# Performance work log

Hardware: AMD Instinct MI355X
Metric: run time of the kernel (lower is better)

## Reference

```python
import jax, jax.numpy as jnp
import numpy as np

B, Z, A = 1024, 512, 8          # batch_size, z_dim, action_dim
AH, ZH = 64, 512                # action_hidden_dim, z_hidden_dim
N_NEG = 100                     # n_neg_actions
TEMP = 0.1                      # temperature
TOP_K = (1, 3, 10)


def forward_model(z, a, Wa, ba, W1, b1, W2, b2):
    # MLP forward model with skip connection (z_delta=True):
    # embed action, concat with z, 2-layer MLP predicting a delta.
    h_a = jax.nn.relu(a @ Wa + ba)                                   # [..., AH]
    h = jax.nn.relu(jnp.concatenate([jnp.broadcast_to(z, a.shape[:-1] + (Z,)), h_a], axis=-1) @ W1 + b1)  # [..., ZH]
    delta = h @ W2 + b2                                              # [..., Z]
    return z + delta


def setup_inputs() -> dict:
    key = jax.random.key(0)
    ks = jax.random.split(key, 8)
    def w(k, shape, fan_in):
        return jax.random.normal(k, shape, jnp.float32) / np.float32(np.sqrt(fan_in))
    z = jax.random.normal(ks[0], (B, Z), jnp.float32)
    z_next = jax.random.normal(ks[1], (B, Z), jnp.float32)
    z_next_hat = jax.random.normal(ks[2], (B, Z), jnp.float32)
    actions = jax.random.normal(ks[3], (B, A), jnp.float32)
    Wa = w(ks[4], (A, AH), A)
    ba = jnp.zeros((AH,), jnp.float32)
    W1 = w(ks[5], (Z + AH, ZH), Z + AH)
    b1 = jnp.zeros((ZH,), jnp.float32)
    W2 = w(ks[6], (ZH, Z), ZH)
    b2 = jnp.zeros((Z,), jnp.float32)
    return {"z": z, "z_next": z_next, "z_next_hat": z_next_hat, "actions": actions,
            "Wa": Wa, "ba": ba, "W1": W1, "b1": b1, "W2": W2, "b2": b2}


def reference(z, z_next, z_next_hat, actions, Wa, ba, W1, b1, W2, b2):
    # ControlCPC.compute_loss with dot_product_similarity, vectorized:
    # the Python loop over n_neg_actions rolled-action forward-model calls
    # becomes one batched [n-1, B, ...] forward-model evaluation.
    batch = z.shape[0]
    n = min(N_NEG, batch)
    sim = z_next @ z_next_hat.T                                      # [B, B] positives on diagonal
    shifts = jnp.arange(1, n)
    neg_actions = jax.vmap(lambda i: jnp.roll(actions, -i, axis=0))(shifts)  # [n-1, B, A]
    z_hat_neg = forward_model(z[None], neg_actions, Wa, ba, W1, b1, W2, b2)  # [n-1, B, Z]
    neg_sim = jnp.einsum('nbz,bz->bn', z_hat_neg, z_next)            # diag of similarity per shift
    sim_mat = jnp.concatenate([sim, neg_sim], axis=1)                # [B, B+n-1]
    # INCE loss, positives on diagonal
    logp = jax.nn.log_softmax(sim_mat / jnp.float32(TEMP), axis=1)
    loss = -jnp.mean(jnp.diagonal(logp))                             # diagonal takes first B entries
    labels = jnp.arange(batch)[:, None]
    accs = []
    for k in TOP_K:
        _, preds = jax.lax.top_k(sim_mat, k)                         # [B, k]
        accs.append(jnp.mean((preds == labels).astype(jnp.float32)) * k)
    return (loss, accs[0], accs[1], accs[2])
```

## Files before the change

kernel.cpp:

```cpp
#include <hip/hip_runtime.h>
#include <math.h>

#define B_SZ 1024
#define Z_DIM 512
#define A_DIM 8
#define AH 64
#define ZH 512
#define NNEG 99
#define INV_T 10.0f

typedef __attribute__((ext_vector_type(8))) short short8;
typedef __attribute__((ext_vector_type(4))) float f32x4;

__device__ __forceinline__ void cvt8(float4 x0, float4 x1, short8& hi, short8& lo) {
    float xs[8] = {x0.x, x0.y, x0.z, x0.w, x1.x, x1.y, x1.z, x1.w};
#pragma unroll
    for (int i = 0; i < 8; ++i) {
        unsigned uu = __float_as_uint(xs[i]);
        hi[i] = (short)(uu >> 16);
        float hf = __uint_as_float(uu & 0xffff0000u);
        lo[i] = (short)(__float_as_uint(xs[i] - hf) >> 16);
    }
}

__device__ __forceinline__ int sw(int m, int kb) { return m * 8 + (kb ^ (m & 7)); }

__global__ __launch_bounds__(256) void prep_kernel(
    const float* __restrict__ W1, const float* __restrict__ actions,
    const float* __restrict__ Wa, const float* __restrict__ ba,
    float* __restrict__ W1T, float* __restrict__ ha, unsigned* __restrict__ cnt)
{
    const int id = blockIdx.x, tid = threadIdx.x;
    if (id == 0 && tid == 0) atomicExch(cnt, 0u);
    if (id < 72) {
        __shared__ float L[64][68];
        int kt = id >> 3, nt = id & 7;
#pragma unroll
        for (int i = 0; i < 4; ++i) {
            int f = tid + i * 256;
            int r = f >> 4, c4 = (f & 15) << 2;
            *(float4*)&L[r][c4] = *(const float4*)&W1[(kt * 64 + r) * 512 + nt * 64 + c4];
        }
        __syncthreads();
#pragma unroll
        for (int i = 0; i < 4; ++i) {
            int f = tid + i * 256;
            int r = f >> 4, c4 = (f & 15) << 2;
            float4 o = {L[c4][r], L[c4 + 1][r], L[c4 + 2][r], L[c4 + 3][r]};
            *(float4*)&W1T[(nt * 64 + r) * 576 + kt * 64 + c4] = o;
        }
    } else if (id < 88) {
        __shared__ float sWa[A_DIM * 64];
        __shared__ float sba[64];
        __shared__ float sact[64][A_DIM];
        int j0 = (id - 72) * 64;
        for (int i = tid; i < A_DIM * 64; i += 256) sWa[i] = Wa[i];
        if (tid < 64) sba[tid] = ba[tid];
        for (int i = tid; i < 64 * A_DIM; i += 256) (&sact[0][0])[i] = actions[j0 * A_DIM + i];
        __syncthreads();
        int r = tid >> 2, c0 = (tid & 3) * 16;
        float o[16];
#pragma unroll
        for (int c = 0; c < 16; ++c) o[c] = sba[c0 + c];
#pragma unroll
        for (int k = 0; k < A_DIM; ++k) {
            float a = sact[r][k];
#pragma unroll
            for (int c = 0; c < 16; ++c) o[c] += a * sWa[k * 64 + c0 + c];
        }
#pragma unroll
        for (int c = 0; c < 16; c += 4) {
            float4 v4 = {fmaxf(o[c], 0.f), fmaxf(o[c + 1], 0.f),
                         fmaxf(o[c + 2], 0.f), fmaxf(o[c + 3], 0.f)};
            *(float4*)&ha[(j0 + r) * 64 + c0 + c] = v4;
        }
    }
}

__global__ __launch_bounds__(256) void mm_kernel(
    const float* __restrict__ z, const float* __restrict__ z_next,
    const float* __restrict__ z_next_hat, const float* __restrict__ W1T,
    const float* __restrict__ b1, const float* __restrict__ W2,
    const float* __restrict__ ha,
    float* __restrict__ sim, float* __restrict__ u, float* __restrict__ v,
    float* __restrict__ g)
{
    __shared__ short Ah[4096], Al[4096], Bh[4096], Bl[4096];

    const int id = blockIdx.x;
    const int tid = threadIdx.x;

    const float* Aop; const float* Bop; const float* bias = nullptr;
    float* C; int N, K, lda, ldb, bm0, bn0;
    if (id < 256) {
        int t = id; bn0 = (t & 15) * 64; bm0 = (t >> 4) * 64;
        Aop = z_next; lda = 512; Bop = z_next_hat; ldb = 512;
        C = sim; N = 1024; K = 512;
    } else if (id < 384) {
        int t = id - 256; bn0 = (t & 7) * 64; bm0 = (t >> 3) * 64;
        Aop = z; lda = 512; Bop = W1T; ldb = 576;
        C = u; N = 512; K = 512; bias = b1;
    } else if (id < 512) {
        int t = id - 384; bn0 = (t & 7) * 64; bm0 = (t >> 3) * 64;
        Aop = z_next; lda = 512; Bop = W2; ldb = 512;
        C = v; N = 512; K = 512;
    } else {
        int t = id - 512; bn0 = (t & 7) * 64; bm0 = (t >> 3) * 64;
        Aop = ha; lda = 64; Bop = W1T + 512; ldb = 576;
        C = g; N = 512; K = 64;
    }

    const int lane = tid & 63, wv = tid >> 6;
    const int lm = lane & 15, lq = lane >> 4;
    const int wm = (wv >> 1) * 32, wn = (wv & 1) * 32;
    const int sr = tid >> 2, sq = tid & 3;
    short8* Ah8 = (short8*)Ah; short8* Al8 = (short8*)Al;
    short8* Bh8 = (short8*)Bh; short8* Bl8 = (short8*)Bl;
    f32x4 acc[2][2] = {};

    for (int k0 = 0; k0 < K; k0 += 64) {
        {
            const float* base = &Aop[(bm0 + sr) * lda + k0 + sq * 16];
            float4 x0 = *(const float4*)(base + 0), x1 = *(const float4*)(base + 4);
            float4 x2 = *(const float4*)(base + 8), x3 = *(const float4*)(base + 12);
            short8 h, l;
            cvt8(x0, x1, h, l); Ah8[sw(sr, 2 * sq)] = h;     Al8[sw(sr, 2 * sq)] = l;
            cvt8(x2, x3, h, l); Ah8[sw(sr, 2 * sq + 1)] = h; Al8[sw(sr, 2 * sq + 1)] = l;
        }
        {
            const float* base = &Bop[(bn0 + sr) * ldb + k0 + sq * 16];
            float4 x0 = *(const float4*)(base + 0), x1 = *(const float4*)(base + 4);
            float4 x2 = *(const float4*)(base + 8), x3 = *(const float4*)(base + 12);
            short8 h, l;
            cvt8(x0, x1, h, l); Bh8[sw(sr, 2 * sq)] = h;     Bl8[sw(sr, 2 * sq)] = l;
            cvt8(x2, x3, h, l); Bh8[sw(sr, 2 * sq + 1)] = h; Bl8[sw(sr, 2 * sq + 1)] = l;
        }
        __syncthreads();
#pragma unroll
        for (int kk = 0; kk < 64; kk += 32) {
            int kbi = (kk >> 3) + lq;
            short8 ah[2], al[2], bh[2], bl[2];
#pragma unroll
            for (int i = 0; i < 2; ++i) {
                ah[i] = Ah8[sw(wm + i * 16 + lm, kbi)];
                al[i] = Al8[sw(wm + i * 16 + lm, kbi)];
                bh[i] = Bh8[sw(wn + i * 16 + lm, kbi)];
                bl[i] = Bl8[sw(wn + i * 16 + lm, kbi)];
            }
#pragma unroll
            for (int i = 0; i < 2; ++i)
#pragma unroll
                for (int j = 0; j < 2; ++j) {
                    acc[i][j] = __builtin_amdgcn_mfma_f32_16x16x32_bf16(ah[i], bh[j], acc[i][j], 0, 0, 0);
                    acc[i][j] = __builtin_amdgcn_mfma_f32_16x16x32_bf16(ah[i], bl[j], acc[i][j], 0, 0, 0);
                    acc[i][j] = __builtin_amdgcn_mfma_f32_16x16x32_bf16(al[i], bh[j], acc[i][j], 0, 0, 0);
                }
        }
        __syncthreads();
    }
#pragma unroll
    for (int i = 0; i < 2; ++i)
#pragma unroll
        for (int j = 0; j < 2; ++j) {
            int n = bn0 + wn + j * 16 + lm;
            float bb = bias ? bias[n] : 0.0f;
#pragma unroll
            for (int r = 0; r < 4; ++r) {
                int m = bm0 + wm + i * 16 + lq * 4 + r;
                C[m * N + n] = acc[i][j][r] + bb;
            }
        }
}

__global__ __launch_bounds__(256) void row2_kernel(
    const float* __restrict__ sim, const float* __restrict__ u,
    const float* __restrict__ v, const float* __restrict__ g,
    const float* __restrict__ z, const float* __restrict__ z_next,
    const float* __restrict__ b2,
    float* __restrict__ pw, unsigned* __restrict__ cnt, float* __restrict__ out)
{
    const int blk = blockIdx.x;
    const int tid = threadIdx.x;
    const int w = tid >> 6, lane = tid & 63;
    const int b = blk * 4 + w;
    __shared__ float gbuf[8][512];
    __shared__ float rn[4][100];
    __shared__ float sacc[4][4];
    __shared__ float red[256];
    __shared__ int sdone;

    float4 ua = *(const float4*)&u[b * 512 + lane * 4];
    float4 ub = *(const float4*)&u[b * 512 + 256 + lane * 4];
    float4 va = *(const float4*)&v[b * 512 + lane * 4];
    float4 vb = *(const float4*)&v[b * 512 + 256 + lane * 4];

    float p;
    {
        float4 za = *(const float4*)&z[b * 512 + lane * 4];
        float4 zb = *(const float4*)&z[b * 512 + 256 + lane * 4];
        float4 na = *(const float4*)&z_next[b * 512 + lane * 4];
        float4 nb = *(const float4*)&z_next[b * 512 + 256 + lane * 4];
        float4 ca = *(const float4*)&b2[lane * 4];
        float4 cb = *(const float4*)&b2[256 + lane * 4];
        p  = (za.x + ca.x) * na.x + (za.y + ca.y) * na.y + (za.z + ca.z) * na.z + (za.w + ca.w) * na.w;
        p += (zb.x + cb.x) * nb.x + (zb.y + cb.y) * nb.y + (zb.z + cb.z) * nb.z + (zb.w + cb.w) * nb.w;
    }
    for (int off = 32; off; off >>= 1) p += __shfl_down(p, off);
    float c0 = __shfl(p, 0);

    const int J0 = blk * 4;
    for (int it = 0; it < 13; ++it) {
#pragma unroll
        for (int ph = 0; ph < 4; ++ph) {
            int f4i = tid + ph * 256;
            int row = f4i >> 7, c = f4i & 127;
            int idx = it * 8 + row;
            if (idx < 102) {
                int jr = (J0 + 1 + idx) & (B_SZ - 1);
                *(float4*)&gbuf[row][c * 4] = *(const float4*)&g[jr * 512 + c * 4];
            }
        }
        __syncthreads();
        float d[8];
#pragma unroll
        for (int ri = 0; ri < 8; ++ri) {
            float4 g0 = *(const float4*)&gbuf[ri][lane * 4];
            float4 g1 = *(const float4*)&gbuf[ri][256 + lane * 4];
            float t = 0.0f;
            t += fmaxf(ua.x + g0.x, 0.0f) * va.x;
            t += fmaxf(ua.y + g0.y, 0.0f) * va.y;
            t += fmaxf(ua.z + g0.z, 0.0f) * va.z;
            t += fmaxf(ua.w + g0.w, 0.0f) * va.w;
            t += fmaxf(ub.x + g1.x, 0.0f) * vb.x;
            t += fmaxf(ub.y + g1.y, 0.0f) * vb.y;
            t += fmaxf(ub.z + g1.z, 0.0f) * vb.z;
            t += fmaxf(ub.w + g1.w, 0.0f) * vb.w;
            d[ri] = t;
        }
        for (int off = 32; off; off >>= 1) {
#pragma unroll
            for (int ri = 0; ri < 8; ++ri) d[ri] += __shfl_down(d[ri], off);
        }
        if (lane == 0) {
#pragma unroll
            for (int ri = 0; ri < 8; ++ri) {
                int idx = it * 8 + ri;
                int s1 = idx - w;
                if (idx < 102 && s1 >= 0 && s1 < 99) rn[w][s1] = c0 + d[ri];
            }
        }
        __syncthreads();
    }

    float4 sv[4];
#pragma unroll
    for (int i = 0; i < 4; ++i)
        sv[i] = *(const float4*)&sim[b * 1024 + lane * 16 + i * 4];
    float nva = rn[w][lane];
    float nvb = (lane < 35) ? rn[w][lane + 64] : -3.4e38f;
    float diag = sim[b * 1024 + b];

    float m = fmaxf(nva, nvb);
#pragma unroll
    for (int i = 0; i < 4; ++i)
        m = fmaxf(m, fmaxf(fmaxf(sv[i].x, sv[i].y), fmaxf(sv[i].z, sv[i].w)));
    for (int off = 32; off; off >>= 1) m = fmaxf(m, __shfl_xor(m, off));

    float es = 0.0f; int ck = 0;
#pragma unroll
    for (int i = 0; i < 4; ++i) {
        float xs[4] = {sv[i].x, sv[i].y, sv[i].z, sv[i].w};
#pragma unroll
        for (int c = 0; c < 4; ++c) {
            int j = lane * 16 + i * 4 + c;
            float x = xs[c];
            es += __expf((x - m) * INV_T);
            if (x > diag) ck++;
            else if (j < b && x == diag) ck++;
        }
    }
    es += __expf((nva - m) * INV_T);
    if (nva > diag) ck++;
    if (lane < 35) {
        es += __expf((nvb - m) * INV_T);
        if (nvb > diag) ck++;
    }
    for (int off = 32; off; off >>= 1) {
        es += __shfl_down(es, off);
        ck += __shfl_down(ck, off);
    }
    if (lane == 0) {
        float loss_b = (m - diag) * INV_T + logf(es);
        sacc[w][0] = loss_b;
        sacc[w][1] = (ck < 1) ? 1.0f : 0.0f;
        sacc[w][2] = (ck < 3) ? 1.0f : 0.0f;
        sacc[w][3] = (ck < 10) ? 1.0f : 0.0f;
    }
    __syncthreads();
    if (tid == 0) {
#pragma unroll
        for (int c = 0; c < 4; ++c)
            pw[blk * 4 + c] = sacc[0][c] + sacc[1][c] + sacc[2][c] + sacc[3][c];
        __threadfence();
        unsigned old = atomicAdd(cnt, 1u);
        sdone = (old == 255u) ? 1 : 0;
    }
    __syncthreads();
    if (sdone) {
        __threadfence();
        int c = tid & 3;
        float s = 0.0f;
        for (int r = tid >> 2; r < 256; r += 64) s += pw[r * 4 + c];
        red[tid] = s;
        __syncthreads();
        if (tid < 4) {
            float t = 0.0f;
            for (int q = 0; q < 64; ++q) t += red[tid + q * 4];
            out[tid] = t * (1.0f / (float)B_SZ);
        }
    }
}

extern "C" void kernel_launch(void* const* d_in, const int* in_sizes, int n_in,
                              void* d_out, int out_size, void* d_ws, size_t ws_size,
                              hipStream_t stream) {
    const float* z          = (const float*)d_in[0];
    const float* z_next     = (const float*)d_in[1];
    const float* z_next_hat = (const float*)d_in[2];
    const float* actions    = (const float*)d_in[3];
    const float* Wa         = (const float*)d_in[4];
    const float* ba         = (const float*)d_in[5];
    const float* W1         = (const float*)d_in[6];
    const float* b1         = (const float*)d_in[7];
    const float* W2         = (const float*)d_in[8];
    const float* b2         = (const float*)d_in[9];
    float* out = (float*)d_out;

    float* ws   = (float*)d_ws;
    float* sim  = ws;
    float* u    = sim + B_SZ * B_SZ;
    float* v    = u + B_SZ * ZH;
    float* g    = v + B_SZ * ZH;
    float* W1T  = g + B_SZ * ZH;
    float* ha   = W1T + 512 * 576;
    float* pw   = ha + B_SZ * AH;
    unsigned* cnt = (unsigned*)(pw + 256 * 4);

    prep_kernel<<<88, 256, 0, stream>>>(W1, actions, Wa, ba, W1T, ha, cnt);
    mm_kernel<<<640, 256, 0, stream>>>(z, z_next, z_next_hat, W1T, b1, W2, ha,
                                       sim, u, v, g);
    row2_kernel<<<256, 256, 0, stream>>>(sim, u, v, g, z, z_next, b2, pw, cnt, out);
}
```

Measured before the change: 124.1 us.

## Use single-pass bf16 MFMA and split row reduction across two wave halves

Replaces the hi/lo split-bf16 GEMM (three MFMAs per tile) with a single round-to-nearest bf16 MFMA. This cuts matrix work and LDS traffic to about a third, and the staging tiles to half. The row kernel now runs 512 threads per block, so each row's 512-wide dot products are split across two wave groups and the partial results are combined in shared memory. The cost is lower GEMM precision, which can change near-tied similarity rankings in the top-k accuracy, plus extra block-level barriers in the row kernel.

```diff
diff --git a/kernel.cpp b/kernel.cpp
--- a/kernel.cpp
+++ b/kernel.cpp
@@ -12,15 +12,14 @@
 typedef __attribute__((ext_vector_type(8))) short short8;
 typedef __attribute__((ext_vector_type(4))) float f32x4;
 
-__device__ __forceinline__ void cvt8(float4 x0, float4 x1, short8& hi, short8& lo) {
-    float xs[8] = {x0.x, x0.y, x0.z, x0.w, x1.x, x1.y, x1.z, x1.w};
-#pragma unroll
-    for (int i = 0; i < 8; ++i) {
-        unsigned uu = __float_as_uint(xs[i]);
-        hi[i] = (short)(uu >> 16);
-        float hf = __uint_as_float(uu & 0xffff0000u);
-        lo[i] = (short)(__float_as_uint(xs[i] - hf) >> 16);
-    }
+__device__ __forceinline__ short bf16rn(float x) {
+    unsigned u = __float_as_uint(x);
+    u += 0x7fffu + ((u >> 16) & 1u);
+    return (short)(u >> 16);
+}
+__device__ __forceinline__ void cvt8rn(float4 x0, float4 x1, short8& h) {
+    h[0] = bf16rn(x0.x); h[1] = bf16rn(x0.y); h[2] = bf16rn(x0.z); h[3] = bf16rn(x0.w);
+    h[4] = bf16rn(x1.x); h[5] = bf16rn(x1.y); h[6] = bf16rn(x1.z); h[7] = bf16rn(x1.w);
 }
 
 __device__ __forceinline__ int sw(int m, int kb) { return m * 8 + (kb ^ (m & 7)); }
@@ -85,7 +84,7 @@
     float* __restrict__ sim, float* __restrict__ u, float* __restrict__ v,
     float* __restrict__ g)
 {
-    __shared__ short Ah[4096], Al[4096], Bh[4096], Bl[4096];
+    __shared__ short Ah[4096], Bh[4096];
 
     const int id = blockIdx.x;
     const int tid = threadIdx.x;
@@ -114,8 +113,7 @@
     const int lm = lane & 15, lq = lane >> 4;
     const int wm = (wv >> 1) * 32, wn = (wv & 1) * 32;
     const int sr = tid >> 2, sq = tid & 3;
-    short8* Ah8 = (short8*)Ah; short8* Al8 = (short8*)Al;
-    short8* Bh8 = (short8*)Bh; short8* Bl8 = (short8*)Bl;
+    short8* Ah8 = (short8*)Ah; short8* Bh8 = (short8*)Bh;
     f32x4 acc[2][2] = {};
 
     for (int k0 = 0; k0 < K; k0 += 64) {
@@ -123,38 +121,33 @@
             const float* base = &Aop[(bm0 + sr) * lda + k0 + sq * 16];
             float4 x0 = *(const float4*)(base + 0), x1 = *(const float4*)(base + 4);
             float4 x2 = *(const float4*)(base + 8), x3 = *(const float4*)(base + 12);
-            short8 h, l;
-            cvt8(x0, x1, h, l); Ah8[sw(sr, 2 * sq)] = h;     Al8[sw(sr, 2 * sq)] = l;
-            cvt8(x2, x3, h, l); Ah8[sw(sr, 2 * sq + 1)] = h; Al8[sw(sr, 2 * sq + 1)] = l;
+            short8 h;
+            cvt8rn(x0, x1, h); Ah8[sw(sr, 2 * sq)] = h;
+            cvt8rn(x2, x3, h); Ah8[sw(sr, 2 * sq + 1)] = h;
         }
         {
             const float* base = &Bop[(bn0 + sr) * ldb + k0 + sq * 16];
             float4 x0 = *(const float4*)(base + 0), x1 = *(const float4*)(base + 4);
             float4 x2 = *(const float4*)(base + 8), x3 = *(const float4*)(base + 12);
-            short8 h, l;
-            cvt8(x0, x1, h, l); Bh8[sw(sr, 2 * sq)] = h;     Bl8[sw(sr, 2 * sq)] = l;
-            cvt8(x2, x3, h, l); Bh8[sw(sr, 2 * sq + 1)] = h; Bl8[sw(sr, 2 * sq + 1)] = l;
+            short8 h;
+            cvt8rn(x0, x1, h); Bh8[sw(sr, 2 * sq)] = h;
+            cvt8rn(x2, x3, h); Bh8[sw(sr, 2 * sq + 1)] = h;
         }
         __syncthreads();
 #pragma unroll
         for (int kk = 0; kk < 64; kk += 32) {
             int kbi = (kk >> 3) + lq;
-            short8 ah[2], al[2], bh[2], bl[2];
+            short8 ah[2], bh[2];
 #pragma unroll
             for (int i = 0; i < 2; ++i) {
                 ah[i] = Ah8[sw(wm + i * 16 + lm, kbi)];
-                al[i] = Al8[sw(wm + i * 16 + lm, kbi)];
                 bh[i] = Bh8[sw(wn + i * 16 + lm, kbi)];
-                bl[i] = Bl8[sw(wn + i * 16 + lm, kbi)];
             }
 #pragma unroll
             for (int i = 0; i < 2; ++i)
 #pragma unroll
-                for (int j = 0; j < 2; ++j) {
+                for (int j = 0; j < 2; ++j)
                     acc[i][j] = __builtin_amdgcn_mfma_f32_16x16x32_bf16(ah[i], bh[j], acc[i][j], 0, 0, 0);
-                    acc[i][j] = __builtin_amdgcn_mfma_f32_16x16x32_bf16(ah[i], bl[j], acc[i][j], 0, 0, 0);
-                    acc[i][j] = __builtin_amdgcn_mfma_f32_16x16x32_bf16(al[i], bh[j], acc[i][j], 0, 0, 0);
-                }
         }
         __syncthreads();
     }
@@ -172,7 +165,7 @@
         }
 }
 
-__global__ __launch_bounds__(256) void row2_kernel(
+__global__ __launch_bounds__(512) void row2_kernel(
     const float* __restrict__ sim, const float* __restrict__ u,
     const float* __restrict__ v, const float* __restrict__ g,
     const float* __restrict__ z, const float* __restrict__ z_next,
@@ -182,37 +175,39 @@
     const int blk = blockIdx.x;
     const int tid = threadIdx.x;
     const int w = tid >> 6, lane = tid & 63;
-    const int b = blk * 4 + w;
+    const int w4 = w & 3, kh = w >> 2;
+    const int b = blk * 4 + w4;
     __shared__ float gbuf[8][512];
     __shared__ float rn[4][100];
+    __shared__ float spart[8][8];
+    __shared__ float c0p[8];
+    __shared__ float mpart[8], espart[8];
+    __shared__ int ckpart[8];
     __shared__ float sacc[4][4];
     __shared__ float red[256];
     __shared__ int sdone;
 
-    float4 ua = *(const float4*)&u[b * 512 + lane * 4];
-    float4 ub = *(const float4*)&u[b * 512 + 256 + lane * 4];
-    float4 va = *(const float4*)&v[b * 512 + lane * 4];
-    float4 vb = *(const float4*)&v[b * 512 + 256 + lane * 4];
-
-    float p;
+    const int base = b * 512 + kh * 256 + lane * 4;
+    const float4 ua = *(const float4*)&u[base];
+    const float4 va = *(const float4*)&v[base];
+
     {
-        float4 za = *(const float4*)&z[b * 512 + lane * 4];
-        float4 zb = *(const float4*)&z[b * 512 + 256 + lane * 4];
-        float4 na = *(const float4*)&z_next[b * 512 + lane * 4];
-        float4 nb = *(const float4*)&z_next[b * 512 + 256 + lane * 4];
-        float4 ca = *(const float4*)&b2[lane * 4];
-        float4 cb = *(const float4*)&b2[256 + lane * 4];
-        p  = (za.x + ca.x) * na.x + (za.y + ca.y) * na.y + (za.z + ca.z) * na.z + (za.w + ca.w) * na.w;
-        p += (zb.x + cb.x) * nb.x + (zb.y + cb.y) * nb.y + (zb.z + cb.z) * nb.z + (zb.w + cb.w) * nb.w;
-    }
-    for (int off = 32; off; off >>= 1) p += __shfl_down(p, off);
-    float c0 = __shfl(p, 0);
+        float4 za = *(const float4*)&z[base];
+        float4 na = *(const float4*)&z_next[base];
+        float4 ca = *(const float4*)&b2[kh * 256 + lane * 4];
+        float p = (za.x + ca.x) * na.x + (za.y + ca.y) * na.y
+                + (za.z + ca.z) * na.z + (za.w + ca.w) * na.w;
+        for (int off = 32; off; off >>= 1) p += __shfl_down(p, off);
+        if (lane == 0) c0p[w] = p;
+    }
+    __syncthreads();
+    const float c0 = c0p[w4] + c0p[w4 + 4];
 
     const int J0 = blk * 4;
     for (int it = 0; it < 13; ++it) {
 #pragma unroll
-        for (int ph = 0; ph < 4; ++ph) {
-            int f4i = tid + ph * 256;
+        for (int ph = 0; ph < 2; ++ph) {
+            int f4i = tid + ph * 512;
             int row = f4i >> 7, c = f4i & 127;
             int idx = it * 8 + row;
             if (idx < 102) {
@@ -224,17 +219,12 @@
         float d[8];
 #pragma unroll
         for (int ri = 0; ri < 8; ++ri) {
-            float4 g0 = *(const float4*)&gbuf[ri][lane * 4];
-            float4 g1 = *(const float4*)&gbuf[ri][256 + lane * 4];
+            float4 g0 = *(const float4*)&gbuf[ri][kh * 256 + lane * 4];
             float t = 0.0f;
             t += fmaxf(ua.x + g0.x, 0.0f) * va.x;
             t += fmaxf(ua.y + g0.y, 0.0f) * va.y;
             t += fmaxf(ua.z + g0.z, 0.0f) * va.z;
             t += fmaxf(ua.w + g0.w, 0.0f) * va.w;
-            t += fmaxf(ub.x + g1.x, 0.0f) * vb.x;
-            t += fmaxf(ub.y + g1.y, 0.0f) * vb.y;
-            t += fmaxf(ub.z + g1.z, 0.0f) * vb.z;
-            t += fmaxf(ub.w + g1.w, 0.0f) * vb.w;
             d[ri] = t;
         }
         for (int off = 32; off; off >>= 1) {
@@ -243,58 +233,70 @@
         }
         if (lane == 0) {
 #pragma unroll
-            for (int ri = 0; ri < 8; ++ri) {
-                int idx = it * 8 + ri;
-                int s1 = idx - w;
-                if (idx < 102 && s1 >= 0 && s1 < 99) rn[w][s1] = c0 + d[ri];
-            }
-        }
-        __syncthreads();
-    }
-
-    float4 sv[4];
-#pragma unroll
-    for (int i = 0; i < 4; ++i)
-        sv[i] = *(const float4*)&sim[b * 1024 + lane * 16 + i * 4];
-    float nva = rn[w][lane];
-    float nvb = (lane < 35) ? rn[w][lane + 64] : -3.4e38f;
+            for (int ri = 0; ri < 8; ++ri) spart[w][ri] = d[ri];
+        }
+        __syncthreads();
+        if (w < 4 && lane < 8) {
+            int idx = it * 8 + lane;
+            int s1 = idx - w;
+            if (idx < 102 && s1 >= 0 && s1 < 99)
+                rn[w][s1] = c0 + spart[w][lane] + spart[w + 4][lane];
+        }
+        __syncthreads();
+    }
+
+    const int j0 = kh * 512 + lane * 8;
+    float4 s0 = *(const float4*)&sim[b * 1024 + j0];
+    float4 s1v = *(const float4*)&sim[b * 1024 + j0 + 4];
     float diag = sim[b * 1024 + b];
+    float nva = -3.4e38f, nvb = -3.4e38f;
+    if (kh == 1) {
+        nva = rn[w4][lane];
+        if (lane < 35) nvb = rn[w4][lane + 64];
+    }
 
     float m = fmaxf(nva, nvb);
-#pragma unroll
-    for (int i = 0; i < 4; ++i)
-        m = fmaxf(m, fmaxf(fmaxf(sv[i].x, sv[i].y), fmaxf(sv[i].z, sv[i].w)));
+    m = fmaxf(m, fmaxf(fmaxf(s0.x, s0.y), fmaxf(s0.z, s0.w)));
+    m = fmaxf(m, fmaxf(fmaxf(s1v.x, s1v.y), fmaxf(s1v.z, s1v.w)));
     for (int off = 32; off; off >>= 1) m = fmaxf(m, __shfl_xor(m, off));
+    if (lane == 0) mpart[w] = m;
+    __syncthreads();
+    m = fmaxf(mpart[w4], mpart[w4 + 4]);
 
     float es = 0.0f; int ck = 0;
-#pragma unroll
-    for (int i = 0; i < 4; ++i) {
-        float xs[4] = {sv[i].x, sv[i].y, sv[i].z, sv[i].w};
-#pragma unroll
-        for (int c = 0; c < 4; ++c) {
-            int j = lane * 16 + i * 4 + c;
+    {
+        float xs[8] = {s0.x, s0.y, s0.z, s0.w, s1v.x, s1v.y, s1v.z, s1v.w};
+#pragma unroll
+        for (int c = 0; c < 8; ++c) {
+            int j = j0 + c;
             float x = xs[c];
             es += __expf((x - m) * INV_T);
             if (x > diag) ck++;
             else if (j < b && x == diag) ck++;
         }
     }
-    es += __expf((nva - m) * INV_T);
-    if (nva > diag) ck++;
-    if (lane < 35) {
-        es += __expf((nvb - m) * INV_T);
-        if (nvb > diag) ck++;
+    if (kh == 1) {
+        es += __expf((nva - m) * INV_T);
+        if (nva > diag) ck++;
+        if (lane < 35) {
+            es += __expf((nvb - m) * INV_T);
+            if (nvb > diag) ck++;
+        }
     }
     for (int off = 32; off; off >>= 1) {
         es += __shfl_down(es, off);
         ck += __shfl_down(ck, off);
     }
-    if (lane == 0) {
-        float loss_b = (m - diag) * INV_T + logf(es);
+    if (lane == 0) { espart[w] = es; ckpart[w] = ck; }
+    __syncthreads();
+    if (w < 4 && lane == 0) {
+        float est = espart[w] + espart[w + 4];
+        int ckt = ckpart[w] + ckpart[w + 4];
+        float loss_b = (m - diag) * INV_T + logf(est);
         sacc[w][0] = loss_b;
-        sacc[w][1] = (ck < 1) ? 1.0f : 0.0f;
-        sacc[w][2] = (ck < 3) ? 1.0f : 0.0f;
-        sacc[w][3] = (ck < 10) ? 1.0f : 0.0f;
+        sacc[w][1] = (ckt < 1) ? 1.0f : 0.0f;
+        sacc[w][2] = (ckt < 3) ? 1.0f : 0.0f;
+        sacc[w][3] = (ckt < 10) ? 1.0f : 0.0f;
     }
     __syncthreads();
     if (tid == 0) {
@@ -306,7 +308,7 @@
         sdone = (old == 255u) ? 1 : 0;
     }
     __syncthreads();
-    if (sdone) {
+    if (sdone && tid < 256) {
         __threadfence();
         int c = tid & 3;
         float s = 0.0f;
@@ -349,5 +351,5 @@
     prep_kernel<<<88, 256, 0, stream>>>(W1, actions, Wa, ba, W1T, ha, cnt);
     mm_kernel<<<640, 256, 0, stream>>>(z, z_next, z_next_hat, W1T, b1, W2, ha,
                                        sim, u, v, g);
-    row2_kernel<<<256, 256, 0, stream>>>(sim, u, v, g, z, z_next, b2, pw, cnt, out);
-}
+    row2_kernel<<<256, 512, 0, stream>>>(sim, u, v, g, z, z_next, b2, pw, cnt, out);
+}
```

After: 126.5 us. Within noise of the previous version (+2.0%).

## Use single-pass bf16 GEMMs and double-buffer g rows with register prefetch

Applied to the files above, without the earlier changes.

The mm_kernel drops the split hi/lo bf16 emulation of fp32 (three MFMAs per tile) and uses one round-to-nearest bf16 MFMA per tile, halving shared memory and cutting MFMA work threefold. This lowers precision of sim, u, v and g, which can change the top-k accuracies and the loss beyond tolerance. Separately, row2_kernel prefetches the next chunk of g rows into registers and alternates between two shared buffers, removing one barrier per iteration so global loads overlap the dot-product compute.

```diff
diff --git a/kernel.cpp b/kernel.cpp
--- a/kernel.cpp
+++ b/kernel.cpp
@@ -12,15 +12,14 @@
 typedef __attribute__((ext_vector_type(8))) short short8;
 typedef __attribute__((ext_vector_type(4))) float f32x4;
 
-__device__ __forceinline__ void cvt8(float4 x0, float4 x1, short8& hi, short8& lo) {
-    float xs[8] = {x0.x, x0.y, x0.z, x0.w, x1.x, x1.y, x1.z, x1.w};
-#pragma unroll
-    for (int i = 0; i < 8; ++i) {
-        unsigned uu = __float_as_uint(xs[i]);
-        hi[i] = (short)(uu >> 16);
-        float hf = __uint_as_float(uu & 0xffff0000u);
-        lo[i] = (short)(__float_as_uint(xs[i] - hf) >> 16);
-    }
+__device__ __forceinline__ short bf16rn(float x) {
+    unsigned u = __float_as_uint(x);
+    u += 0x7fffu + ((u >> 16) & 1u);
+    return (short)(u >> 16);
+}
+__device__ __forceinline__ void cvt8rn(float4 x0, float4 x1, short8& h) {
+    h[0] = bf16rn(x0.x); h[1] = bf16rn(x0.y); h[2] = bf16rn(x0.z); h[3] = bf16rn(x0.w);
+    h[4] = bf16rn(x1.x); h[5] = bf16rn(x1.y); h[6] = bf16rn(x1.z); h[7] = bf16rn(x1.w);
 }
 
 __device__ __forceinline__ int sw(int m, int kb) { return m * 8 + (kb ^ (m & 7)); }
@@ -85,7 +84,7 @@
     float* __restrict__ sim, float* __restrict__ u, float* __restrict__ v,
     float* __restrict__ g)
 {
-    __shared__ short Ah[4096], Al[4096], Bh[4096], Bl[4096];
+    __shared__ short Ah[4096], Bh[4096];
 
     const int id = blockIdx.x;
     const int tid = threadIdx.x;
@@ -114,8 +113,7 @@
     const int lm = lane & 15, lq = lane >> 4;
     const int wm = (wv >> 1) * 32, wn = (wv & 1) * 32;
     const int sr = tid >> 2, sq = tid & 3;
-    short8* Ah8 = (short8*)Ah; short8* Al8 = (short8*)Al;
-    short8* Bh8 = (short8*)Bh; short8* Bl8 = (short8*)Bl;
+    short8* Ah8 = (short8*)Ah; short8* Bh8 = (short8*)Bh;
     f32x4 acc[2][2] = {};
 
     for (int k0 = 0; k0 < K; k0 += 64) {
@@ -123,38 +121,33 @@
             const float* base = &Aop[(bm0 + sr) * lda + k0 + sq * 16];
             float4 x0 = *(const float4*)(base + 0), x1 = *(const float4*)(base + 4);
             float4 x2 = *(const float4*)(base + 8), x3 = *(const float4*)(base + 12);
-            short8 h, l;
-            cvt8(x0, x1, h, l); Ah8[sw(sr, 2 * sq)] = h;     Al8[sw(sr, 2 * sq)] = l;
-            cvt8(x2, x3, h, l); Ah8[sw(sr, 2 * sq + 1)] = h; Al8[sw(sr, 2 * sq + 1)] = l;
+            short8 h;
+            cvt8rn(x0, x1, h); Ah8[sw(sr, 2 * sq)] = h;
+            cvt8rn(x2, x3, h); Ah8[sw(sr, 2 * sq + 1)] = h;
         }
         {
             const float* base = &Bop[(bn0 + sr) * ldb + k0 + sq * 16];
             float4 x0 = *(const float4*)(base + 0), x1 = *(const float4*)(base + 4);
             float4 x2 = *(const float4*)(base + 8), x3 = *(const float4*)(base + 12);
-            short8 h, l;
-            cvt8(x0, x1, h, l); Bh8[sw(sr, 2 * sq)] = h;     Bl8[sw(sr, 2 * sq)] = l;
-            cvt8(x2, x3, h, l); Bh8[sw(sr, 2 * sq + 1)] = h; Bl8[sw(sr, 2 * sq + 1)] = l;
+            short8 h;
+            cvt8rn(x0, x1, h); Bh8[sw(sr, 2 * sq)] = h;
+            cvt8rn(x2, x3, h); Bh8[sw(sr, 2 * sq + 1)] = h;
         }
         __syncthreads();
 #pragma unroll
         for (int kk = 0; kk < 64; kk += 32) {
             int kbi = (kk >> 3) + lq;
-            short8 ah[2], al[2], bh[2], bl[2];
+            short8 ah[2], bh[2];
 #pragma unroll
             for (int i = 0; i < 2; ++i) {
                 ah[i] = Ah8[sw(wm + i * 16 + lm, kbi)];
-                al[i] = Al8[sw(wm + i * 16 + lm, kbi)];
                 bh[i] = Bh8[sw(wn + i * 16 + lm, kbi)];
-                bl[i] = Bl8[sw(wn + i * 16 + lm, kbi)];
             }
 #pragma unroll
             for (int i = 0; i < 2; ++i)
 #pragma unroll
-                for (int j = 0; j < 2; ++j) {
+                for (int j = 0; j < 2; ++j)
                     acc[i][j] = __builtin_amdgcn_mfma_f32_16x16x32_bf16(ah[i], bh[j], acc[i][j], 0, 0, 0);
-                    acc[i][j] = __builtin_amdgcn_mfma_f32_16x16x32_bf16(ah[i], bl[j], acc[i][j], 0, 0, 0);
-                    acc[i][j] = __builtin_amdgcn_mfma_f32_16x16x32_bf16(al[i], bh[j], acc[i][j], 0, 0, 0);
-                }
         }
         __syncthreads();
     }
@@ -183,7 +176,7 @@
     const int tid = threadIdx.x;
     const int w = tid >> 6, lane = tid & 63;
     const int b = blk * 4 + w;
-    __shared__ float gbuf[8][512];
+    __shared__ float gbuf[2][8][512];
     __shared__ float rn[4][100];
     __shared__ float sacc[4][4];
     __shared__ float red[256];
@@ -206,26 +199,45 @@
         p += (zb.x + cb.x) * nb.x + (zb.y + cb.y) * nb.y + (zb.z + cb.z) * nb.z + (zb.w + cb.w) * nb.w;
     }
     for (int off = 32; off; off >>= 1) p += __shfl_down(p, off);
-    float c0 = __shfl(p, 0);
+    const float c0 = __shfl(p, 0);
 
     const int J0 = blk * 4;
+    const int prow = tid >> 7;
+    (void)prow;
+
+    float4 pre[4];
+#pragma unroll
+    for (int ph = 0; ph < 4; ++ph) {
+        int f4i = tid + ph * 256;
+        int row = f4i >> 7, c = f4i & 127;
+        int jr = (J0 + 1 + row) & (B_SZ - 1);
+        pre[ph] = *(const float4*)&g[jr * 512 + c * 4];
+    }
+
+    int pbuf = 0;
     for (int it = 0; it < 13; ++it) {
 #pragma unroll
         for (int ph = 0; ph < 4; ++ph) {
             int f4i = tid + ph * 256;
             int row = f4i >> 7, c = f4i & 127;
-            int idx = it * 8 + row;
-            if (idx < 102) {
+            *(float4*)&gbuf[pbuf][row][c * 4] = pre[ph];
+        }
+        __syncthreads();
+        if (it < 12) {
+#pragma unroll
+            for (int ph = 0; ph < 4; ++ph) {
+                int f4i = tid + ph * 256;
+                int row = f4i >> 7, c = f4i & 127;
+                int idx = (it + 1) * 8 + row;
                 int jr = (J0 + 1 + idx) & (B_SZ - 1);
-                *(float4*)&gbuf[row][c * 4] = *(const float4*)&g[jr * 512 + c * 4];
+                pre[ph] = *(const float4*)&g[jr * 512 + c * 4];
             }
         }
-        __syncthreads();
         float d[8];
 #pragma unroll
         for (int ri = 0; ri < 8; ++ri) {
-            float4 g0 = *(const float4*)&gbuf[ri][lane * 4];
-            float4 g1 = *(const float4*)&gbuf[ri][256 + lane * 4];
+            float4 g0 = *(const float4*)&gbuf[pbuf][ri][lane * 4];
+            float4 g1 = *(const float4*)&gbuf[pbuf][ri][256 + lane * 4];
             float t = 0.0f;
             t += fmaxf(ua.x + g0.x, 0.0f) * va.x;
             t += fmaxf(ua.y + g0.y, 0.0f) * va.y;
@@ -249,8 +261,9 @@
                 if (idx < 102 && s1 >= 0 && s1 < 99) rn[w][s1] = c0 + d[ri];
             }
         }
-        __syncthreads();
-    }
+        pbuf ^= 1;
+    }
+    __syncthreads();
 
     float4 sv[4];
 #pragma unroll
```

Measured after the change: 128.2 us. 1.03x slower.
